# Optimization experiments

Measured on AMD Instinct MI355X. Metric: run time of the kernel, lower is better.

## Reference

```python
import jax, jax.numpy as jnp
import numpy as np

B, S, H = 4, 2048, 1024
EXP_BITS, SIG_BITS = 5, 10  # rmode=1 -> round-to-nearest


def quantize(x):
    """Simulated low-precision float quantization (LightChop-style) with STE.

    exp_bits exponent bits (bias = 2^(e-1)-1, exponent clamped -> subnormal
    handling falls out of the clamp), sig_bits significand bits, round-to-nearest.
    """
    bias = 2 ** (EXP_BITS - 1) - 1
    ax = jnp.abs(x)
    e = jnp.floor(jnp.log2(jnp.where(ax > 0, ax, 1.0)))
    e = jnp.clip(e, 1 - bias, bias)               # clamp to representable exponent range
    scale = jnp.exp2(e - SIG_BITS)                # ulp at this exponent
    q = jnp.round(x / scale) * scale              # round significand to SIG_BITS bits
    max_val = (2.0 - 2.0 ** (-SIG_BITS)) * 2.0 ** bias
    q = jnp.clip(q, -max_val, max_val)            # saturate overflow
    # straight-through estimator: forward = q, backward = identity
    return x + jax.lax.stop_gradient(q - x)


def setup_inputs() -> dict:
    key = jax.random.key(0)
    ks = jax.random.split(key, 7)
    w_scale = 1.0 / np.sqrt(H)
    return {
        "x": jax.random.normal(ks[0], (B, S, H), dtype=jnp.float32),
        "Wq": jax.random.normal(ks[1], (H, H), dtype=jnp.float32) * w_scale,
        "bq": jax.random.normal(ks[2], (H,), dtype=jnp.float32) * 0.01,
        "Wk": jax.random.normal(ks[3], (H, H), dtype=jnp.float32) * w_scale,
        "bk": jax.random.normal(ks[4], (H,), dtype=jnp.float32) * 0.01,
        "Wv": jax.random.normal(ks[5], (H, H), dtype=jnp.float32) * w_scale,
        "bv": jax.random.normal(ks[6], (H,), dtype=jnp.float32) * 0.01,
    }


def reference(x, Wq, bq, Wk, bk, Wv, bv):
    # nn.Linear: y = x @ W.T + b   (W stored [out, in])
    q = quantize(jnp.einsum("bsh,oh->bso", x, Wq) + bq)
    k = quantize(jnp.einsum("bsh,oh->bso", x, Wk) + bk)
    v = quantize(jnp.einsum("bsh,oh->bso", x, Wv) + bv)
    inv_sqrt_h = 1.0 / (H ** 0.5)
    scores = quantize(jnp.einsum("bsh,bth->bst", q, k) * inv_sqrt_h)  # [B,S,S]
    attn = quantize(jax.nn.softmax(scores, axis=-1))
    return jnp.einsum("bst,bth->bsh", attn, v)
```

## Files before the change

kernel.cpp:

```cpp
#include <hip/hip_runtime.h>
#include <hip/hip_fp16.h>

#define B_ 4
#define S_ 2048
#define H_ 1024
#define M_ (B_ * S_)

typedef _Float16 f16;
typedef _Float16 f16x8 __attribute__((ext_vector_type(8)));
typedef _Float16 f16x4 __attribute__((ext_vector_type(4)));
typedef float f32x4 __attribute__((ext_vector_type(4)));

typedef __attribute__((address_space(3))) unsigned int* lds_u32p;
typedef const __attribute__((address_space(1))) unsigned int* gbl_u32p;

__device__ __forceinline__ void stage16(const f16* g, f16* l) {
  __builtin_amdgcn_global_load_lds((gbl_u32p)g, (lds_u32p)l, 16, 0, 0);
}

__global__ __launch_bounds__(256) void downconvert_all(
    const float* __restrict__ x, const float* __restrict__ W0,
    const float* __restrict__ W1, const float* __restrict__ W2,
    f16* __restrict__ xh, f16* __restrict__ Wh) {
  const int b = blockIdx.x;
  const float* src;
  f16* dst;
  long i;
  if (b < M_ * H_ / 1024) {
    src = x; dst = xh;
    i = (long)b * 256 + threadIdx.x;
  } else {
    const int wb = b - M_ * H_ / 1024;
    const int sel = wb >> 10;
    src = sel == 0 ? W0 : (sel == 1 ? W1 : W2);
    dst = Wh + (long)sel * H_ * H_;
    i = (long)(wb & 1023) * 256 + threadIdx.x;
  }
  f32x4 v = ((const f32x4*)src)[i];
  f16x4 h;
#pragma unroll
  for (int c = 0; c < 4; c++) h[c] = (f16)v[c];
  ((f16x4*)dst)[i] = h;
}

__global__ __launch_bounds__(256, 2)
void qkv_gemm(const f16* __restrict__ xh, const f16* __restrict__ Wh,
              const float* __restrict__ bq, const float* __restrict__ bk,
              const float* __restrict__ bv, f16* __restrict__ qkv,
              f16* __restrict__ vT) {
  __shared__ __align__(16) f16 As[2 * 128 * 32];
  __shared__ __align__(16) f16 Bs[2 * 128 * 32];
  const int t = threadIdx.x;
  const int wave = t >> 6, lane = t & 63;
  const int quad = lane >> 4, l16 = lane & 15;
  const int wm = (wave & 1) * 64, wn = (wave >> 1) * 64;
  const int sel = blockIdx.y >> 3;
  const int ntile = (blockIdx.y & 7) * 128;
  const int mtile = blockIdx.x * 128;

  const f16* Ab = xh + (long)mtile * H_;
  const f16* Bb = Wh + (long)sel * H_ * H_ + (long)ntile * H_;

  const int r0 = t >> 2;
  const int c8 = (t & 3) * 8;

  f32x4 acc[4][4] = {};

  for (int k0 = 0; k0 < H_; k0 += 64) {
    __syncthreads();
    stage16(Ab + (long)r0 * H_ + k0 + c8,             As + t * 8);
    stage16(Ab + (long)(r0 + 64) * H_ + k0 + c8,      As + 2048 + t * 8);
    stage16(Ab + (long)r0 * H_ + k0 + 32 + c8,        As + 4096 + t * 8);
    stage16(Ab + (long)(r0 + 64) * H_ + k0 + 32 + c8, As + 6144 + t * 8);
    stage16(Bb + (long)r0 * H_ + k0 + c8,             Bs + t * 8);
    stage16(Bb + (long)(r0 + 64) * H_ + k0 + c8,      Bs + 2048 + t * 8);
    stage16(Bb + (long)r0 * H_ + k0 + 32 + c8,        Bs + 4096 + t * 8);
    stage16(Bb + (long)(r0 + 64) * H_ + k0 + 32 + c8, Bs + 6144 + t * 8);
    __syncthreads();
#pragma unroll
    for (int kk = 0; kk < 2; kk++) {
      f16x8 ah[4], bh[4];
#pragma unroll
      for (int i = 0; i < 4; i++) {
        ah[i] = *(const f16x8*)&As[kk * 4096 + (wm + i * 16 + l16) * 32 + quad * 8];
        bh[i] = *(const f16x8*)&Bs[kk * 4096 + (wn + i * 16 + l16) * 32 + quad * 8];
      }
#pragma unroll
      for (int i = 0; i < 4; i++)
#pragma unroll
        for (int j = 0; j < 4; j++)
          acc[i][j] = __builtin_amdgcn_mfma_f32_16x16x32_f16(ah[i], bh[j], acc[i][j], 0, 0, 0);
    }
  }

  const float* bias = sel == 0 ? bq : (sel == 1 ? bk : bv);
  if (sel == 2) {
#pragma unroll
    for (int j = 0; j < 4; j++) {
      int n = ntile + wn + j * 16 + l16;
      float bb = bias[n];
#pragma unroll
      for (int i = 0; i < 4; i++) {
        int m = mtile + wm + i * 16 + quad * 4;
        f16x4 pack;
#pragma unroll
        for (int r = 0; r < 4; r++) pack[r] = (f16)(acc[i][j][r] + bb);
        *(f16x4*)&vT[((long)(m >> 11) * H_ + n) * S_ + (m & 2047)] = pack;
      }
    }
  } else {
    f16* out = qkv + (long)sel * M_ * H_;
#pragma unroll
    for (int j = 0; j < 4; j++) {
      int n = ntile + wn + j * 16 + l16;
      float bb = bias[n];
#pragma unroll
      for (int i = 0; i < 4; i++) {
        int m = mtile + wm + i * 16 + quad * 4;
#pragma unroll
        for (int r = 0; r < 4; r++)
          out[(long)(m + r) * H_ + n] = (f16)(acc[i][j][r] + bb);
      }
    }
  }
}

template <int OUT_F16>
__global__ __launch_bounds__(256, 2)
void gemm_nt(const f16* __restrict__ A, const f16* __restrict__ Bm,
             void* __restrict__ C, int lda, int ldb, int ldc, int K,
             long sA, long sB, long sC, float alpha) {
  __shared__ __align__(16) f16 As[2 * 128 * 32];
  __shared__ __align__(16) f16 Bs[2 * 128 * 32];
  const int t = threadIdx.x;
  const int wave = t >> 6, lane = t & 63;
  const int quad = lane >> 4, l16 = lane & 15;
  const int wm = (wave & 1) * 64, wn = (wave >> 1) * 64;
  const f16* Ab = A + blockIdx.z * sA + (long)blockIdx.x * 128 * lda;
  const f16* Bb = Bm + blockIdx.z * sB + (long)blockIdx.y * 128 * ldb;
  const int r0 = t >> 2, c8 = (t & 3) * 8;
  f32x4 acc[4][4] = {};
  for (int k0 = 0; k0 < K; k0 += 64) {
    __syncthreads();
    stage16(Ab + (long)r0 * lda + k0 + c8,             As + t * 8);
    stage16(Ab + (long)(r0 + 64) * lda + k0 + c8,      As + 2048 + t * 8);
    stage16(Ab + (long)r0 * lda + k0 + 32 + c8,        As + 4096 + t * 8);
    stage16(Ab + (long)(r0 + 64) * lda + k0 + 32 + c8, As + 6144 + t * 8);
    stage16(Bb + (long)r0 * ldb + k0 + c8,             Bs + t * 8);
    stage16(Bb + (long)(r0 + 64) * ldb + k0 + c8,      Bs + 2048 + t * 8);
    stage16(Bb + (long)r0 * ldb + k0 + 32 + c8,        Bs + 4096 + t * 8);
    stage16(Bb + (long)(r0 + 64) * ldb + k0 + 32 + c8, Bs + 6144 + t * 8);
    __syncthreads();
#pragma unroll
    for (int kk = 0; kk < 2; kk++) {
      f16x8 af[4], bf[4];
#pragma unroll
      for (int i = 0; i < 4; i++) {
        af[i] = *(const f16x8*)&As[kk * 4096 + (wm + i * 16 + l16) * 32 + quad * 8];
        bf[i] = *(const f16x8*)&Bs[kk * 4096 + (wn + i * 16 + l16) * 32 + quad * 8];
      }
#pragma unroll
      for (int i = 0; i < 4; i++)
#pragma unroll
        for (int j = 0; j < 4; j++)
          acc[i][j] = __builtin_amdgcn_mfma_f32_16x16x32_f16(af[i], bf[j], acc[i][j], 0, 0, 0);
    }
  }
  const long mb = (long)blockIdx.x * 128 + wm;
  const long nb = (long)blockIdx.y * 128 + wn;
#pragma unroll
  for (int i = 0; i < 4; i++)
#pragma unroll
    for (int j = 0; j < 4; j++) {
      long m = mb + i * 16 + quad * 4;
      long n = nb + j * 16 + l16;
#pragma unroll
      for (int r = 0; r < 4; r++) {
        float v = acc[i][j][r] * alpha;
        if (OUT_F16)
          ((f16*)C)[blockIdx.z * sC + (m + r) * ldc + n] = (f16)v;
        else
          ((float*)C)[blockIdx.z * sC + (m + r) * ldc + n] = v;
      }
    }
}

__global__ __launch_bounds__(256) void softmax_q(f16* __restrict__ sc) {
  const long row = blockIdx.x;
  f16* p = sc + row * S_;
  const int t = threadIdx.x;
  const int wave = t >> 6, lane = t & 63;
  f16x8 v = ((const f16x8*)p)[t];
  float f[8];
  float m = -3.0e38f;
#pragma unroll
  for (int c = 0; c < 8; c++) { f[c] = (float)v[c]; m = fmaxf(m, f[c]); }
#pragma unroll
  for (int o = 32; o > 0; o >>= 1) m = fmaxf(m, __shfl_xor(m, o));
  __shared__ float redm[4], reds[4];
  if (lane == 0) redm[wave] = m;
  __syncthreads();
  m = fmaxf(fmaxf(redm[0], redm[1]), fmaxf(redm[2], redm[3]));
  float s = 0.f, e[8];
#pragma unroll
  for (int c = 0; c < 8; c++) { e[c] = __expf(f[c] - m); s += e[c]; }
#pragma unroll
  for (int o = 32; o > 0; o >>= 1) s += __shfl_xor(s, o);
  if (lane == 0) reds[wave] = s;
  __syncthreads();
  s = reds[0] + reds[1] + reds[2] + reds[3];
  float inv = 1.0f / s;
  f16x8 ov;
#pragma unroll
  for (int c = 0; c < 8; c++) ov[c] = (f16)(e[c] * inv);
  ((f16x8*)p)[t] = ov;
}

extern "C" void kernel_launch(void* const* d_in, const int* in_sizes, int n_in,
                              void* d_out, int out_size, void* d_ws, size_t ws_size,
                              hipStream_t stream) {
  (void)in_sizes; (void)n_in; (void)out_size; (void)ws_size;
  const float* x  = (const float*)d_in[0];
  const float* Wq = (const float*)d_in[1];
  const float* bq = (const float*)d_in[2];
  const float* Wk = (const float*)d_in[3];
  const float* bk = (const float*)d_in[4];
  const float* Wv = (const float*)d_in[5];
  const float* bv = (const float*)d_in[6];

  char* ws = (char*)d_ws;
  f16* xh  = (f16*)ws; ws += (size_t)M_ * H_ * 2;
  f16* Wh  = (f16*)ws; ws += (size_t)3 * H_ * H_ * 2;
  f16* qkv = (f16*)ws; ws += (size_t)2 * M_ * H_ * 2;
  f16* vT  = (f16*)ws; ws += (size_t)B_ * H_ * S_ * 2;
  f16* sc  = (f16*)ws; ws += (size_t)B_ * S_ * S_ * 2;

  downconvert_all<<<M_ * H_ / 1024 + 3 * H_ * H_ / 1024, 256, 0, stream>>>(
      x, Wq, Wk, Wv, xh, Wh);

  qkv_gemm<<<dim3(64, 24), 256, 0, stream>>>(xh, Wh, bq, bk, bv, qkv, vT);

  gemm_nt<1><<<dim3(16, 16, 4), 256, 0, stream>>>(
      qkv, qkv + (size_t)M_ * H_, sc, H_, H_, S_, H_,
      (long)S_ * H_, (long)S_ * H_, (long)S_ * S_, 0.03125f);

  softmax_q<<<M_, 256, 0, stream>>>(sc);

  gemm_nt<0><<<dim3(16, 8, 4), 256, 0, stream>>>(
      sc, vT, d_out, S_, S_, H_, S_,
      (long)S_ * S_, (long)H_ * S_, (long)S_ * H_, 1.0f);
}
```

Baseline: 248.3 us.

## Replace QKV and score GEMMs with 8-wave 256x256 multi-stage pipelined kernel

Introduces a templated 512-thread GEMM with 256x256 tiles, a 4-buffer LDS ring that prefetches three k-steps ahead via direct global-to-LDS loads, XOR-swizzled LDS layout, split barriers and setprio around MFMA bursts. It replaces both the QKV projection kernel and the QK^T score GEMM. The aim is to hide global load latency, raise data reuse per block and reduce LDS bank conflicts. In exchange it uses much more LDS and registers per block (acc[8][4]), which limits occupancy, and the larger tiles give fewer blocks (384 and 256), so wave quantization on the CUs may get worse.

```diff
diff --git a/kernel.cpp b/kernel.cpp
--- a/kernel.cpp
+++ b/kernel.cpp
@@ -43,83 +43,146 @@
   ((f16x4*)dst)[i] = h;
 }
 
-__global__ __launch_bounds__(256, 2)
-void qkv_gemm(const f16* __restrict__ xh, const f16* __restrict__ Wh,
-              const float* __restrict__ bq, const float* __restrict__ bk,
-              const float* __restrict__ bv, f16* __restrict__ qkv,
-              f16* __restrict__ vT) {
-  __shared__ __align__(16) f16 As[2 * 128 * 32];
-  __shared__ __align__(16) f16 Bs[2 * 128 * 32];
+template <int EPI>
+__global__ __launch_bounds__(512, 2)
+void gemm8p(const f16* __restrict__ A, const f16* __restrict__ Bm,
+            const float* __restrict__ bq, const float* __restrict__ bk,
+            const float* __restrict__ bv, f16* __restrict__ out,
+            f16* __restrict__ vT, float alpha) {
+  __shared__ __align__(16) f16 LA[4][256 * 32];
+  __shared__ __align__(16) f16 LB[4][256 * 32];
   const int t = threadIdx.x;
-  const int wave = t >> 6, lane = t & 63;
+  const int wv = t >> 6, lane = t & 63;
   const int quad = lane >> 4, l16 = lane & 15;
-  const int wm = (wave & 1) * 64, wn = (wave >> 1) * 64;
-  const int sel = blockIdx.y >> 3;
-  const int ntile = (blockIdx.y & 7) * 128;
-  const int mtile = blockIdx.x * 128;
-
-  const f16* Ab = xh + (long)mtile * H_;
-  const f16* Bb = Wh + (long)sel * H_ * H_ + (long)ntile * H_;
-
-  const int r0 = t >> 2;
-  const int c8 = (t & 3) * 8;
-
-  f32x4 acc[4][4] = {};
-
-  for (int k0 = 0; k0 < H_; k0 += 64) {
-    __syncthreads();
-    stage16(Ab + (long)r0 * H_ + k0 + c8,             As + t * 8);
-    stage16(Ab + (long)(r0 + 64) * H_ + k0 + c8,      As + 2048 + t * 8);
-    stage16(Ab + (long)r0 * H_ + k0 + 32 + c8,        As + 4096 + t * 8);
-    stage16(Ab + (long)(r0 + 64) * H_ + k0 + 32 + c8, As + 6144 + t * 8);
-    stage16(Bb + (long)r0 * H_ + k0 + c8,             Bs + t * 8);
-    stage16(Bb + (long)(r0 + 64) * H_ + k0 + c8,      Bs + 2048 + t * 8);
-    stage16(Bb + (long)r0 * H_ + k0 + 32 + c8,        Bs + 4096 + t * 8);
-    stage16(Bb + (long)(r0 + 64) * H_ + k0 + 32 + c8, Bs + 6144 + t * 8);
-    __syncthreads();
-#pragma unroll
-    for (int kk = 0; kk < 2; kk++) {
-      f16x8 ah[4], bh[4];
-#pragma unroll
-      for (int i = 0; i < 4; i++) {
-        ah[i] = *(const f16x8*)&As[kk * 4096 + (wm + i * 16 + l16) * 32 + quad * 8];
-        bh[i] = *(const f16x8*)&Bs[kk * 4096 + (wn + i * 16 + l16) * 32 + quad * 8];
-      }
-#pragma unroll
-      for (int i = 0; i < 4; i++)
-#pragma unroll
-        for (int j = 0; j < 4; j++)
-          acc[i][j] = __builtin_amdgcn_mfma_f32_16x16x32_f16(ah[i], bh[j], acc[i][j], 0, 0, 0);
-    }
-  }
-
-  const float* bias = sel == 0 ? bq : (sel == 1 ? bk : bv);
-  if (sel == 2) {
-#pragma unroll
-    for (int j = 0; j < 4; j++) {
-      int n = ntile + wn + j * 16 + l16;
-      float bb = bias[n];
-#pragma unroll
-      for (int i = 0; i < 4; i++) {
-        int m = mtile + wm + i * 16 + quad * 4;
-        f16x4 pack;
-#pragma unroll
-        for (int r = 0; r < 4; r++) pack[r] = (f16)(acc[i][j][r] + bb);
-        *(f16x4*)&vT[((long)(m >> 11) * H_ + n) * S_ + (m & 2047)] = pack;
-      }
-    }
+  const int wm = (wv >> 2) * 128;
+  const int wn = (wv & 3) * 64;
+
+  int bm, bn, sel = 0;
+  const f16 *Ab, *Bb;
+  if (EPI == 1) {
+    bm = blockIdx.x * 256;
+    sel = blockIdx.y >> 2;
+    bn = (blockIdx.y & 3) * 256;
+    Ab = A + (long)bm * H_;
+    Bb = Bm + (long)sel * H_ * H_ + (long)bn * H_;
   } else {
-    f16* out = qkv + (long)sel * M_ * H_;
-#pragma unroll
-    for (int j = 0; j < 4; j++) {
-      int n = ntile + wn + j * 16 + l16;
-      float bb = bias[n];
-#pragma unroll
-      for (int i = 0; i < 4; i++) {
-        int m = mtile + wm + i * 16 + quad * 4;
-#pragma unroll
-        for (int r = 0; r < 4; r++)
-          out[(long)(m + r) * H_ + n] = (f16)(acc[i][j][r] + bb);
+    bm = blockIdx.x * 256;
+    bn = blockIdx.y * 256;
+    Ab = A + (long)blockIdx.z * S_ * H_ + (long)bm * H_;
+    Bb = Bm + (long)blockIdx.z * S_ * H_ + (long)bn * H_;
+  }
+
+  const int srow = t >> 2;
+  const int sch = (t & 3) ^ ((srow >> 1) & 3);
+  const long goff = (long)srow * H_ + sch * 8;
+  const int loff = t * 8;
+
+  const int swz = quad ^ ((l16 >> 1) & 3);
+  const int aoff = (wm + l16) * 32 + swz * 8;
+  const int boff = (wn + l16) * 32 + swz * 8;
+
+  f32x4 acc[8][4] = {};
+
+#pragma unroll
+  for (int p = 0; p < 3; ++p) {
+    stage16(Ab + goff + p * 32, &LA[p][loff]);
+    stage16(Ab + goff + 128 * H_ + p * 32, &LA[p][loff + 4096]);
+    stage16(Bb + goff + p * 32, &LB[p][loff]);
+    stage16(Bb + goff + 128 * H_ + p * 32, &LB[p][loff + 4096]);
+  }
+
+#define KT_BODY(kt, VM, DO_STAGE)                                             \
+  {                                                                           \
+    asm volatile("s_waitcnt vmcnt(" #VM ")" ::: "memory");                    \
+    __builtin_amdgcn_s_barrier();                                             \
+    const int buf_ = (kt) & 3;                                                \
+    const f16* LAb = LA[buf_];                                                \
+    const f16* LBb = LB[buf_];                                                \
+    f16x8 af[4], bf[4], ag[4];                                                \
+    _Pragma("unroll") for (int mi = 0; mi < 4; ++mi)                          \
+        af[mi] = *(const f16x8*)&LAb[aoff + mi * 512];                        \
+    _Pragma("unroll") for (int ni = 0; ni < 4; ++ni)                          \
+        bf[ni] = *(const f16x8*)&LBb[boff + ni * 512];                        \
+    if (DO_STAGE) {                                                           \
+      stage16(Ab + goff + ((kt) + 3) * 32, &LA[((kt) + 3) & 3][loff]);        \
+      stage16(Ab + goff + 128 * H_ + ((kt) + 3) * 32,                         \
+              &LA[((kt) + 3) & 3][loff + 4096]);                              \
+    }                                                                         \
+    __builtin_amdgcn_s_barrier();                                             \
+    asm volatile("s_waitcnt lgkmcnt(0)" ::: "memory");                        \
+    __builtin_amdgcn_sched_barrier(0);                                        \
+    __builtin_amdgcn_s_setprio(1);                                            \
+    _Pragma("unroll") for (int mi = 0; mi < 4; ++mi)                          \
+        _Pragma("unroll") for (int ni = 0; ni < 4; ++ni)                      \
+            acc[mi][ni] = __builtin_amdgcn_mfma_f32_16x16x32_f16(             \
+                af[mi], bf[ni], acc[mi][ni], 0, 0, 0);                        \
+    __builtin_amdgcn_s_setprio(0);                                            \
+    _Pragma("unroll") for (int mi = 0; mi < 4; ++mi)                          \
+        ag[mi] = *(const f16x8*)&LAb[aoff + 2048 + mi * 512];                 \
+    if (DO_STAGE) {                                                           \
+      stage16(Bb + goff + ((kt) + 3) * 32, &LB[((kt) + 3) & 3][loff]);        \
+      stage16(Bb + goff + 128 * H_ + ((kt) + 3) * 32,                         \
+              &LB[((kt) + 3) & 3][loff + 4096]);                              \
+    }                                                                         \
+    __builtin_amdgcn_s_barrier();                                             \
+    asm volatile("s_waitcnt lgkmcnt(0)" ::: "memory");                        \
+    __builtin_amdgcn_sched_barrier(0);                                        \
+    __builtin_amdgcn_s_setprio(1);                                            \
+    _Pragma("unroll") for (int mi = 0; mi < 4; ++mi)                          \
+        _Pragma("unroll") for (int ni = 0; ni < 4; ++ni)                      \
+            acc[mi + 4][ni] = __builtin_amdgcn_mfma_f32_16x16x32_f16(         \
+                ag[mi], bf[ni], acc[mi + 4][ni], 0, 0, 0);                    \
+    __builtin_amdgcn_s_setprio(0);                                            \
+  }
+
+#pragma unroll 4
+  for (int kt = 0; kt < 29; ++kt) KT_BODY(kt, 8, 1)
+  KT_BODY(29, 8, 0)
+  KT_BODY(30, 4, 0)
+  KT_BODY(31, 0, 0)
+#undef KT_BODY
+
+  if (EPI == 0) {
+    f16* C = out + (long)blockIdx.z * S_ * S_;
+#pragma unroll
+    for (int mi = 0; mi < 8; ++mi)
+#pragma unroll
+      for (int ni = 0; ni < 4; ++ni) {
+        const long m = bm + wm + mi * 16 + quad * 4;
+        const long n = bn + wn + ni * 16 + l16;
+#pragma unroll
+        for (int r = 0; r < 4; ++r)
+          C[(m + r) * S_ + n] = (f16)(acc[mi][ni][r] * alpha);
+      }
+  } else {
+    const float* bias = sel == 0 ? bq : (sel == 1 ? bk : bv);
+    if (sel == 2) {
+#pragma unroll
+      for (int ni = 0; ni < 4; ++ni) {
+        const int n = bn + wn + ni * 16 + l16;
+        const float bb = bias[n];
+#pragma unroll
+        for (int mi = 0; mi < 8; ++mi) {
+          const int m = bm + wm + mi * 16 + quad * 4;
+          f16x4 pack;
+#pragma unroll
+          for (int r = 0; r < 4; ++r) pack[r] = (f16)(acc[mi][ni][r] + bb);
+          *(f16x4*)&vT[((long)(m >> 11) * H_ + n) * S_ + (m & 2047)] = pack;
+        }
+      }
+    } else {
+      f16* C = out + (long)sel * M_ * H_;
+#pragma unroll
+      for (int ni = 0; ni < 4; ++ni) {
+        const int n = bn + wn + ni * 16 + l16;
+        const float bb = bias[n];
+#pragma unroll
+        for (int mi = 0; mi < 8; ++mi) {
+          const long m = bm + wm + mi * 16 + quad * 4;
+#pragma unroll
+          for (int r = 0; r < 4; ++r)
+            C[(m + r) * H_ + n] = (f16)(acc[mi][ni][r] + bb);
+        }
       }
     }
   }
@@ -238,11 +301,12 @@
   downconvert_all<<<M_ * H_ / 1024 + 3 * H_ * H_ / 1024, 256, 0, stream>>>(
       x, Wq, Wk, Wv, xh, Wh);
 
-  qkv_gemm<<<dim3(64, 24), 256, 0, stream>>>(xh, Wh, bq, bk, bv, qkv, vT);
-
-  gemm_nt<1><<<dim3(16, 16, 4), 256, 0, stream>>>(
-      qkv, qkv + (size_t)M_ * H_, sc, H_, H_, S_, H_,
-      (long)S_ * H_, (long)S_ * H_, (long)S_ * S_, 0.03125f);
+  gemm8p<1><<<dim3(32, 12), 512, 0, stream>>>(
+      xh, Wh, bq, bk, bv, qkv, vT, 0.f);
+
+  gemm8p<0><<<dim3(8, 8, 4), 512, 0, stream>>>(
+      qkv, qkv + (size_t)M_ * H_, nullptr, nullptr, nullptr, sc, nullptr,
+      0.03125f);
 
   softmax_q<<<M_, 256, 0, stream>>>(sc);
 
```

Result: slower. 258.5 us (+4.1%).

## Unify GEMMs into triple-buffered pipelined kernel with swizzled LDS layout

Applied to the files above, without the earlier changes.

Replaces the separate QKV and NT GEMM kernels with one templated kernel. It uses a three-stage LDS ring buffer with a K-step of 32, so global-to-LDS loads for future tiles overlap the MFMA work on the current tile, paced by explicit vmcnt waits and raw barriers. LDS chunks are XOR-swizzled to reduce bank conflicts on the fragment reads, and MFMA sections run at raised wave priority. Occupancy is raised to 3 blocks per CU, which increases register pressure, and the hand-written waitcnt logic is fragile.

```diff
diff --git a/kernel.cpp b/kernel.cpp
--- a/kernel.cpp
+++ b/kernel.cpp
@@ -43,146 +43,176 @@
   ((f16x4*)dst)[i] = h;
 }
 
-__global__ __launch_bounds__(256, 2)
-void qkv_gemm(const f16* __restrict__ xh, const f16* __restrict__ Wh,
-              const float* __restrict__ bq, const float* __restrict__ bk,
-              const float* __restrict__ bv, f16* __restrict__ qkv,
-              f16* __restrict__ vT) {
-  __shared__ __align__(16) f16 As[2 * 128 * 32];
-  __shared__ __align__(16) f16 Bs[2 * 128 * 32];
+template <int KTOT, int EPI>
+__global__ __launch_bounds__(256, 3)
+void gemm_p(const f16* __restrict__ A, const f16* __restrict__ Bm,
+            void* __restrict__ Cout, f16* __restrict__ vT,
+            const float* __restrict__ bq, const float* __restrict__ bk,
+            const float* __restrict__ bv,
+            int lda, int ldb, int ldc, long sA, long sB, long sC,
+            float alpha) {
+  __shared__ __align__(16) f16 LA[3][128 * 32];
+  __shared__ __align__(16) f16 LB[3][128 * 32];
   const int t = threadIdx.x;
   const int wave = t >> 6, lane = t & 63;
   const int quad = lane >> 4, l16 = lane & 15;
   const int wm = (wave & 1) * 64, wn = (wave >> 1) * 64;
-  const int sel = blockIdx.y >> 3;
-  const int ntile = (blockIdx.y & 7) * 128;
-  const int mtile = blockIdx.x * 128;
-
-  const f16* Ab = xh + (long)mtile * H_;
-  const f16* Bb = Wh + (long)sel * H_ * H_ + (long)ntile * H_;
-
-  const int r0 = t >> 2;
-  const int c8 = (t & 3) * 8;
+
+  int sel = 0, ntile = 0, mtile = blockIdx.x * 128;
+  const f16 *Ab, *Bb;
+  if (EPI == 2) {
+    sel = blockIdx.y >> 3;
+    ntile = (blockIdx.y & 7) * 128;
+    Ab = A + (long)mtile * lda;
+    Bb = Bm + (long)sel * H_ * H_ + (long)ntile * ldb;
+  } else {
+    ntile = blockIdx.y * 128;
+    Ab = A + blockIdx.z * sA + (long)mtile * lda;
+    Bb = Bm + blockIdx.z * sB + (long)ntile * ldb;
+  }
+
+  const int srow = t >> 2;
+  const int sch = (t & 3) ^ ((srow >> 1) & 3);
+  const long ga = (long)srow * lda + sch * 8;
+  const long gb = (long)srow * ldb + sch * 8;
+
+  const int swz8 = (quad ^ ((l16 >> 1) & 3)) * 8;
+  const int aoff = (wm + l16) * 32 + swz8;
+  const int boff = (wn + l16) * 32 + swz8;
 
   f32x4 acc[4][4] = {};
 
-  for (int k0 = 0; k0 < H_; k0 += 64) {
-    __syncthreads();
-    stage16(Ab + (long)r0 * H_ + k0 + c8,             As + t * 8);
-    stage16(Ab + (long)(r0 + 64) * H_ + k0 + c8,      As + 2048 + t * 8);
-    stage16(Ab + (long)r0 * H_ + k0 + 32 + c8,        As + 4096 + t * 8);
-    stage16(Ab + (long)(r0 + 64) * H_ + k0 + 32 + c8, As + 6144 + t * 8);
-    stage16(Bb + (long)r0 * H_ + k0 + c8,             Bs + t * 8);
-    stage16(Bb + (long)(r0 + 64) * H_ + k0 + c8,      Bs + 2048 + t * 8);
-    stage16(Bb + (long)r0 * H_ + k0 + 32 + c8,        Bs + 4096 + t * 8);
-    stage16(Bb + (long)(r0 + 64) * H_ + k0 + 32 + c8, Bs + 6144 + t * 8);
-    __syncthreads();
-#pragma unroll
-    for (int kk = 0; kk < 2; kk++) {
-      f16x8 ah[4], bh[4];
-#pragma unroll
-      for (int i = 0; i < 4; i++) {
-        ah[i] = *(const f16x8*)&As[kk * 4096 + (wm + i * 16 + l16) * 32 + quad * 8];
-        bh[i] = *(const f16x8*)&Bs[kk * 4096 + (wn + i * 16 + l16) * 32 + quad * 8];
-      }
-#pragma unroll
-      for (int i = 0; i < 4; i++)
-#pragma unroll
-        for (int j = 0; j < 4; j++)
-          acc[i][j] = __builtin_amdgcn_mfma_f32_16x16x32_f16(ah[i], bh[j], acc[i][j], 0, 0, 0);
+#pragma unroll
+  for (int p = 0; p < 2; ++p) {
+    stage16(Ab + ga + p * 32,                    &LA[p][t * 8]);
+    stage16(Ab + ga + (long)64 * lda + p * 32,   &LA[p][t * 8 + 2048]);
+    stage16(Bb + gb + p * 32,                    &LB[p][t * 8]);
+    stage16(Bb + gb + (long)64 * ldb + p * 32,   &LB[p][t * 8 + 2048]);
+  }
+
+  constexpr int NT = KTOT / 32;
+  int rb = 0, sb = 2;
+  long kg = 64;
+
+#pragma unroll 3
+  for (int kt = 0; kt < NT - 2; ++kt) {
+    asm volatile("s_waitcnt vmcnt(4)" ::: "memory");
+    __builtin_amdgcn_s_barrier();
+    const f16* LAb = &LA[rb][0];
+    const f16* LBb = &LB[rb][0];
+    f16x8 af[4], bf[4];
+#pragma unroll
+    for (int i = 0; i < 4; ++i) {
+      af[i] = *(const f16x8*)&LAb[aoff + i * 512];
+      bf[i] = *(const f16x8*)&LBb[boff + i * 512];
     }
-  }
-
-  const float* bias = sel == 0 ? bq : (sel == 1 ? bk : bv);
-  if (sel == 2) {
-#pragma unroll
-    for (int j = 0; j < 4; j++) {
-      int n = ntile + wn + j * 16 + l16;
-      float bb = bias[n];
-#pragma unroll
-      for (int i = 0; i < 4; i++) {
-        int m = mtile + wm + i * 16 + quad * 4;
-        f16x4 pack;
-#pragma unroll
-        for (int r = 0; r < 4; r++) pack[r] = (f16)(acc[i][j][r] + bb);
-        *(f16x4*)&vT[((long)(m >> 11) * H_ + n) * S_ + (m & 2047)] = pack;
-      }
+    f16* sa = &LA[sb][0];
+    f16* sbb = &LB[sb][0];
+    stage16(Ab + ga + kg,                  sa + t * 8);
+    stage16(Ab + ga + (long)64 * lda + kg, sa + t * 8 + 2048);
+    stage16(Bb + gb + kg,                  sbb + t * 8);
+    stage16(Bb + gb + (long)64 * ldb + kg, sbb + t * 8 + 2048);
+    __builtin_amdgcn_s_barrier();
+    asm volatile("s_waitcnt lgkmcnt(0)" ::: "memory");
+    __builtin_amdgcn_sched_barrier(0);
+    __builtin_amdgcn_s_setprio(1);
+#pragma unroll
+    for (int i = 0; i < 4; ++i)
+#pragma unroll
+      for (int j = 0; j < 4; ++j)
+        acc[i][j] = __builtin_amdgcn_mfma_f32_16x16x32_f16(af[i], bf[j],
+                                                           acc[i][j], 0, 0, 0);
+    __builtin_amdgcn_s_setprio(0);
+    kg += 32;
+    rb = rb == 2 ? 0 : rb + 1;
+    sb = sb == 2 ? 0 : sb + 1;
+  }
+
+#pragma unroll
+  for (int tp = 0; tp < 2; ++tp) {
+    if (tp == 0)
+      asm volatile("s_waitcnt vmcnt(4)" ::: "memory");
+    else
+      asm volatile("s_waitcnt vmcnt(0)" ::: "memory");
+    __builtin_amdgcn_s_barrier();
+    const f16* LAb = &LA[rb][0];
+    const f16* LBb = &LB[rb][0];
+    f16x8 af[4], bf[4];
+#pragma unroll
+    for (int i = 0; i < 4; ++i) {
+      af[i] = *(const f16x8*)&LAb[aoff + i * 512];
+      bf[i] = *(const f16x8*)&LBb[boff + i * 512];
     }
+    __builtin_amdgcn_s_barrier();
+    asm volatile("s_waitcnt lgkmcnt(0)" ::: "memory");
+    __builtin_amdgcn_sched_barrier(0);
+    __builtin_amdgcn_s_setprio(1);
+#pragma unroll
+    for (int i = 0; i < 4; ++i)
+#pragma unroll
+      for (int j = 0; j < 4; ++j)
+        acc[i][j] = __builtin_amdgcn_mfma_f32_16x16x32_f16(af[i], bf[j],
+                                                           acc[i][j], 0, 0, 0);
+    __builtin_amdgcn_s_setprio(0);
+    rb = rb == 2 ? 0 : rb + 1;
+  }
+
+  if (EPI == 0) {
+    f16* C = (f16*)Cout + blockIdx.z * sC;
+#pragma unroll
+    for (int i = 0; i < 4; ++i)
+#pragma unroll
+      for (int j = 0; j < 4; ++j) {
+        const long m = mtile + wm + i * 16 + quad * 4;
+        const long n = ntile + wn + j * 16 + l16;
+#pragma unroll
+        for (int r = 0; r < 4; ++r)
+          C[(m + r) * ldc + n] = (f16)(acc[i][j][r] * alpha);
+      }
+  } else if (EPI == 1) {
+    float* C = (float*)Cout + blockIdx.z * sC;
+#pragma unroll
+    for (int i = 0; i < 4; ++i)
+#pragma unroll
+      for (int j = 0; j < 4; ++j) {
+        const long m = mtile + wm + i * 16 + quad * 4;
+        const long n = ntile + wn + j * 16 + l16;
+#pragma unroll
+        for (int r = 0; r < 4; ++r)
+          C[(m + r) * ldc + n] = acc[i][j][r] * alpha;
+      }
   } else {
-    f16* out = qkv + (long)sel * M_ * H_;
-#pragma unroll
-    for (int j = 0; j < 4; j++) {
-      int n = ntile + wn + j * 16 + l16;
-      float bb = bias[n];
-#pragma unroll
-      for (int i = 0; i < 4; i++) {
-        int m = mtile + wm + i * 16 + quad * 4;
-#pragma unroll
-        for (int r = 0; r < 4; r++)
-          out[(long)(m + r) * H_ + n] = (f16)(acc[i][j][r] + bb);
+    const float* bias = sel == 0 ? bq : (sel == 1 ? bk : bv);
+    if (sel == 2) {
+#pragma unroll
+      for (int j = 0; j < 4; ++j) {
+        const int n = ntile + wn + j * 16 + l16;
+        const float bb = bias[n];
+#pragma unroll
+        for (int i = 0; i < 4; ++i) {
+          const int m = mtile + wm + i * 16 + quad * 4;
+          f16x4 pack;
+#pragma unroll
+          for (int r = 0; r < 4; ++r) pack[r] = (f16)(acc[i][j][r] + bb);
+          *(f16x4*)&vT[((long)(m >> 11) * H_ + n) * S_ + (m & 2047)] = pack;
+        }
+      }
+    } else {
+      f16* C = (f16*)Cout + (long)sel * M_ * H_;
+#pragma unroll
+      for (int j = 0; j < 4; ++j) {
+        const int n = ntile + wn + j * 16 + l16;
+        const float bb = bias[n];
+#pragma unroll
+        for (int i = 0; i < 4; ++i) {
+          const long m = mtile + wm + i * 16 + quad * 4;
+#pragma unroll
+          for (int r = 0; r < 4; ++r)
+            C[(m + r) * ldc + n] = (f16)(acc[i][j][r] + bb);
+        }
       }
     }
   }
-}
-
-template <int OUT_F16>
-__global__ __launch_bounds__(256, 2)
-void gemm_nt(const f16* __restrict__ A, const f16* __restrict__ Bm,
-             void* __restrict__ C, int lda, int ldb, int ldc, int K,
-             long sA, long sB, long sC, float alpha) {
-  __shared__ __align__(16) f16 As[2 * 128 * 32];
-  __shared__ __align__(16) f16 Bs[2 * 128 * 32];
-  const int t = threadIdx.x;
-  const int wave = t >> 6, lane = t & 63;
-  const int quad = lane >> 4, l16 = lane & 15;
-  const int wm = (wave & 1) * 64, wn = (wave >> 1) * 64;
-  const f16* Ab = A + blockIdx.z * sA + (long)blockIdx.x * 128 * lda;
-  const f16* Bb = Bm + blockIdx.z * sB + (long)blockIdx.y * 128 * ldb;
-  const int r0 = t >> 2, c8 = (t & 3) * 8;
-  f32x4 acc[4][4] = {};
-  for (int k0 = 0; k0 < K; k0 += 64) {
-    __syncthreads();
-    stage16(Ab + (long)r0 * lda + k0 + c8,             As + t * 8);
-    stage16(Ab + (long)(r0 + 64) * lda + k0 + c8,      As + 2048 + t * 8);
-    stage16(Ab + (long)r0 * lda + k0 + 32 + c8,        As + 4096 + t * 8);
-    stage16(Ab + (long)(r0 + 64) * lda + k0 + 32 + c8, As + 6144 + t * 8);
-    stage16(Bb + (long)r0 * ldb + k0 + c8,             Bs + t * 8);
-    stage16(Bb + (long)(r0 + 64) * ldb + k0 + c8,      Bs + 2048 + t * 8);
-    stage16(Bb + (long)r0 * ldb + k0 + 32 + c8,        Bs + 4096 + t * 8);
-    stage16(Bb + (long)(r0 + 64) * ldb + k0 + 32 + c8, Bs + 6144 + t * 8);
-    __syncthreads();
-#pragma unroll
-    for (int kk = 0; kk < 2; kk++) {
-      f16x8 af[4], bf[4];
-#pragma unroll
-      for (int i = 0; i < 4; i++) {
-        af[i] = *(const f16x8*)&As[kk * 4096 + (wm + i * 16 + l16) * 32 + quad * 8];
-        bf[i] = *(const f16x8*)&Bs[kk * 4096 + (wn + i * 16 + l16) * 32 + quad * 8];
-      }
-#pragma unroll
-      for (int i = 0; i < 4; i++)
-#pragma unroll
-        for (int j = 0; j < 4; j++)
-          acc[i][j] = __builtin_amdgcn_mfma_f32_16x16x32_f16(af[i], bf[j], acc[i][j], 0, 0, 0);
-    }
-  }
-  const long mb = (long)blockIdx.x * 128 + wm;
-  const long nb = (long)blockIdx.y * 128 + wn;
-#pragma unroll
-  for (int i = 0; i < 4; i++)
-#pragma unroll
-    for (int j = 0; j < 4; j++) {
-      long m = mb + i * 16 + quad * 4;
-      long n = nb + j * 16 + l16;
-#pragma unroll
-      for (int r = 0; r < 4; r++) {
-        float v = acc[i][j][r] * alpha;
-        if (OUT_F16)
-          ((f16*)C)[blockIdx.z * sC + (m + r) * ldc + n] = (f16)v;
-        else
-          ((float*)C)[blockIdx.z * sC + (m + r) * ldc + n] = v;
-      }
-    }
 }
 
 __global__ __launch_bounds__(256) void softmax_q(f16* __restrict__ sc) {
@@ -238,15 +268,16 @@
   downconvert_all<<<M_ * H_ / 1024 + 3 * H_ * H_ / 1024, 256, 0, stream>>>(
       x, Wq, Wk, Wv, xh, Wh);
 
-  qkv_gemm<<<dim3(64, 24), 256, 0, stream>>>(xh, Wh, bq, bk, bv, qkv, vT);
-
-  gemm_nt<1><<<dim3(16, 16, 4), 256, 0, stream>>>(
-      qkv, qkv + (size_t)M_ * H_, sc, H_, H_, S_, H_,
-      (long)S_ * H_, (long)S_ * H_, (long)S_ * S_, 0.03125f);
+  gemm_p<1024, 2><<<dim3(64, 24), 256, 0, stream>>>(
+      xh, Wh, qkv, vT, bq, bk, bv, H_, H_, H_, 0, 0, 0, 0.f);
+
+  gemm_p<1024, 0><<<dim3(16, 16, 4), 256, 0, stream>>>(
+      qkv, qkv + (size_t)M_ * H_, sc, nullptr, nullptr, nullptr, nullptr,
+      H_, H_, S_, (long)S_ * H_, (long)S_ * H_, (long)S_ * S_, 0.03125f);
 
   softmax_q<<<M_, 256, 0, stream>>>(sc);
 
-  gemm_nt<0><<<dim3(16, 8, 4), 256, 0, stream>>>(
-      sc, vT, d_out, S_, S_, H_, S_,
-      (long)S_ * S_, (long)H_ * S_, (long)S_ * H_, 1.0f);
-}
+  gemm_p<2048, 1><<<dim3(16, 8, 4), 256, 0, stream>>>(
+      sc, vT, d_out, nullptr, nullptr, nullptr, nullptr,
+      S_, S_, H_, (long)S_ * S_, (long)H_ * S_, (long)S_ * H_, 1.0f);
+}
```

Result: slower. 262.2 us (+5.6%).

## Use 2-wave 128x64-per-wave GEMM tiles with swizzled LDS for QKV and scores

Applied to the files above, without the earlier changes.

Replaces the QKV projection kernel and the scores GEMM with one templated kernel. It runs 128 threads per block, and each wave computes a 128x64 output tile with 8x4 MFMA accumulators, so every B fragment loaded from LDS is reused across more MFMAs. LDS chunks are XOR-swizzled on the global-to-LDS store and the fragment reads to reduce bank conflicts. In exchange, each wave holds many more accumulator registers and each CU has fewer waves to hide latency.

```diff
diff --git a/kernel.cpp b/kernel.cpp
--- a/kernel.cpp
+++ b/kernel.cpp
@@ -43,83 +43,125 @@
   ((f16x4*)dst)[i] = h;
 }
 
-__global__ __launch_bounds__(256, 2)
-void qkv_gemm(const f16* __restrict__ xh, const f16* __restrict__ Wh,
-              const float* __restrict__ bq, const float* __restrict__ bk,
-              const float* __restrict__ bv, f16* __restrict__ qkv,
-              f16* __restrict__ vT) {
-  __shared__ __align__(16) f16 As[2 * 128 * 32];
-  __shared__ __align__(16) f16 Bs[2 * 128 * 32];
+template <int KTOT, int EPI>
+__global__ __launch_bounds__(128, 2)
+void gemm_f(const f16* __restrict__ A, const f16* __restrict__ Bm,
+            void* __restrict__ Cout, f16* __restrict__ vT,
+            const float* __restrict__ bq, const float* __restrict__ bk,
+            const float* __restrict__ bv,
+            int lda, int ldb, int ldc, long sA, long sB, long sC,
+            float alpha) {
+  __shared__ __align__(16) f16 As[2][128 * 32];
+  __shared__ __align__(16) f16 Bs[2][128 * 32];
   const int t = threadIdx.x;
   const int wave = t >> 6, lane = t & 63;
   const int quad = lane >> 4, l16 = lane & 15;
-  const int wm = (wave & 1) * 64, wn = (wave >> 1) * 64;
-  const int sel = blockIdx.y >> 3;
-  const int ntile = (blockIdx.y & 7) * 128;
-  const int mtile = blockIdx.x * 128;
-
-  const f16* Ab = xh + (long)mtile * H_;
-  const f16* Bb = Wh + (long)sel * H_ * H_ + (long)ntile * H_;
-
-  const int r0 = t >> 2;
-  const int c8 = (t & 3) * 8;
-
-  f32x4 acc[4][4] = {};
-
-  for (int k0 = 0; k0 < H_; k0 += 64) {
-    __syncthreads();
-    stage16(Ab + (long)r0 * H_ + k0 + c8,             As + t * 8);
-    stage16(Ab + (long)(r0 + 64) * H_ + k0 + c8,      As + 2048 + t * 8);
-    stage16(Ab + (long)r0 * H_ + k0 + 32 + c8,        As + 4096 + t * 8);
-    stage16(Ab + (long)(r0 + 64) * H_ + k0 + 32 + c8, As + 6144 + t * 8);
-    stage16(Bb + (long)r0 * H_ + k0 + c8,             Bs + t * 8);
-    stage16(Bb + (long)(r0 + 64) * H_ + k0 + c8,      Bs + 2048 + t * 8);
-    stage16(Bb + (long)r0 * H_ + k0 + 32 + c8,        Bs + 4096 + t * 8);
-    stage16(Bb + (long)(r0 + 64) * H_ + k0 + 32 + c8, Bs + 6144 + t * 8);
-    __syncthreads();
-#pragma unroll
-    for (int kk = 0; kk < 2; kk++) {
-      f16x8 ah[4], bh[4];
-#pragma unroll
-      for (int i = 0; i < 4; i++) {
-        ah[i] = *(const f16x8*)&As[kk * 4096 + (wm + i * 16 + l16) * 32 + quad * 8];
-        bh[i] = *(const f16x8*)&Bs[kk * 4096 + (wn + i * 16 + l16) * 32 + quad * 8];
-      }
-#pragma unroll
-      for (int i = 0; i < 4; i++)
-#pragma unroll
-        for (int j = 0; j < 4; j++)
-          acc[i][j] = __builtin_amdgcn_mfma_f32_16x16x32_f16(ah[i], bh[j], acc[i][j], 0, 0, 0);
-    }
-  }
-
-  const float* bias = sel == 0 ? bq : (sel == 1 ? bk : bv);
-  if (sel == 2) {
-#pragma unroll
-    for (int j = 0; j < 4; j++) {
-      int n = ntile + wn + j * 16 + l16;
-      float bb = bias[n];
-#pragma unroll
-      for (int i = 0; i < 4; i++) {
-        int m = mtile + wm + i * 16 + quad * 4;
-        f16x4 pack;
-#pragma unroll
-        for (int r = 0; r < 4; r++) pack[r] = (f16)(acc[i][j][r] + bb);
-        *(f16x4*)&vT[((long)(m >> 11) * H_ + n) * S_ + (m & 2047)] = pack;
-      }
-    }
+  const int wn = wave * 64;
+
+  int sel = 0, ntile = 0, mtile = blockIdx.x * 128;
+  const f16 *Ab, *Bb;
+  if (EPI == 2) {
+    sel = blockIdx.y >> 3;
+    ntile = (blockIdx.y & 7) * 128;
+    Ab = A + (long)mtile * lda;
+    Bb = Bm + (long)sel * H_ * H_ + (long)ntile * ldb;
   } else {
-    f16* out = qkv + (long)sel * M_ * H_;
-#pragma unroll
-    for (int j = 0; j < 4; j++) {
-      int n = ntile + wn + j * 16 + l16;
-      float bb = bias[n];
-#pragma unroll
-      for (int i = 0; i < 4; i++) {
-        int m = mtile + wm + i * 16 + quad * 4;
-#pragma unroll
-        for (int r = 0; r < 4; r++)
-          out[(long)(m + r) * H_ + n] = (f16)(acc[i][j][r] + bb);
+    ntile = blockIdx.y * 128;
+    Ab = A + blockIdx.z * sA + (long)mtile * lda;
+    Bb = Bm + blockIdx.z * sB + (long)ntile * ldb;
+  }
+
+  const int srow = t >> 2;
+  const int sch = (t & 3) ^ ((t >> 3) & 3);
+  const long gaBase = (long)srow * lda + sch * 8;
+  const long gbBase = (long)srow * ldb + sch * 8;
+
+  const int swz8 = (quad ^ ((l16 >> 1) & 3)) * 8;
+  const int aoff = l16 * 32 + swz8;
+  const int boff = (wn + l16) * 32 + swz8;
+
+  f32x4 acc[8][4] = {};
+
+  for (int k0 = 0; k0 < KTOT; k0 += 64) {
+    __syncthreads();
+#pragma unroll
+    for (int j = 0; j < 4; ++j) {
+      const long rA = gaBase + (long)(32 * j) * lda + k0;
+      const long rB = gbBase + (long)(32 * j) * ldb + k0;
+      stage16(Ab + rA,      &As[0][j * 1024 + t * 8]);
+      stage16(Ab + rA + 32, &As[1][j * 1024 + t * 8]);
+      stage16(Bb + rB,      &Bs[0][j * 1024 + t * 8]);
+      stage16(Bb + rB + 32, &Bs[1][j * 1024 + t * 8]);
+    }
+    __syncthreads();
+#pragma unroll
+    for (int kk = 0; kk < 2; ++kk) {
+      f16x8 af[4], bf[4];
+#pragma unroll
+      for (int i = 0; i < 4; ++i) {
+        af[i] = *(const f16x8*)&As[kk][aoff + i * 512];
+        bf[i] = *(const f16x8*)&Bs[kk][boff + i * 512];
+      }
+#pragma unroll
+      for (int i = 0; i < 4; ++i)
+#pragma unroll
+        for (int j2 = 0; j2 < 4; ++j2)
+          acc[i][j2] = __builtin_amdgcn_mfma_f32_16x16x32_f16(
+              af[i], bf[j2], acc[i][j2], 0, 0, 0);
+      f16x8 ag[4];
+#pragma unroll
+      for (int i = 0; i < 4; ++i)
+        ag[i] = *(const f16x8*)&As[kk][aoff + (i + 4) * 512];
+#pragma unroll
+      for (int i = 0; i < 4; ++i)
+#pragma unroll
+        for (int j2 = 0; j2 < 4; ++j2)
+          acc[i + 4][j2] = __builtin_amdgcn_mfma_f32_16x16x32_f16(
+              ag[i], bf[j2], acc[i + 4][j2], 0, 0, 0);
+    }
+  }
+
+  if (EPI == 0) {
+    f16* C = (f16*)Cout + blockIdx.z * sC;
+#pragma unroll
+    for (int mi = 0; mi < 8; ++mi)
+#pragma unroll
+      for (int ni = 0; ni < 4; ++ni) {
+        const long m = mtile + mi * 16 + quad * 4;
+        const long n = ntile + wn + ni * 16 + l16;
+#pragma unroll
+        for (int r = 0; r < 4; ++r)
+          C[(m + r) * ldc + n] = (f16)(acc[mi][ni][r] * alpha);
+      }
+  } else {
+    const float* bias = sel == 0 ? bq : (sel == 1 ? bk : bv);
+    if (sel == 2) {
+#pragma unroll
+      for (int ni = 0; ni < 4; ++ni) {
+        const int n = ntile + wn + ni * 16 + l16;
+        const float bb = bias[n];
+#pragma unroll
+        for (int mi = 0; mi < 8; ++mi) {
+          const int m = mtile + mi * 16 + quad * 4;
+          f16x4 pack;
+#pragma unroll
+          for (int r = 0; r < 4; ++r) pack[r] = (f16)(acc[mi][ni][r] + bb);
+          *(f16x4*)&vT[((long)(m >> 11) * H_ + n) * S_ + (m & 2047)] = pack;
+        }
+      }
+    } else {
+      f16* C = (f16*)Cout + (long)sel * M_ * H_;
+#pragma unroll
+      for (int ni = 0; ni < 4; ++ni) {
+        const int n = ntile + wn + ni * 16 + l16;
+        const float bb = bias[n];
+#pragma unroll
+        for (int mi = 0; mi < 8; ++mi) {
+          const long m = mtile + mi * 16 + quad * 4;
+#pragma unroll
+          for (int r = 0; r < 4; ++r)
+            C[(m + r) * ldc + n] = (f16)(acc[mi][ni][r] + bb);
+        }
       }
     }
   }
@@ -238,11 +280,12 @@
   downconvert_all<<<M_ * H_ / 1024 + 3 * H_ * H_ / 1024, 256, 0, stream>>>(
       x, Wq, Wk, Wv, xh, Wh);
 
-  qkv_gemm<<<dim3(64, 24), 256, 0, stream>>>(xh, Wh, bq, bk, bv, qkv, vT);
-
-  gemm_nt<1><<<dim3(16, 16, 4), 256, 0, stream>>>(
-      qkv, qkv + (size_t)M_ * H_, sc, H_, H_, S_, H_,
-      (long)S_ * H_, (long)S_ * H_, (long)S_ * S_, 0.03125f);
+  gemm_f<1024, 2><<<dim3(64, 24), 128, 0, stream>>>(
+      xh, Wh, qkv, vT, bq, bk, bv, H_, H_, H_, 0, 0, 0, 0.f);
+
+  gemm_f<1024, 0><<<dim3(16, 16, 4), 128, 0, stream>>>(
+      qkv, qkv + (size_t)M_ * H_, sc, nullptr, nullptr, nullptr, nullptr,
+      H_, H_, S_, (long)S_ * H_, (long)S_ * H_, (long)S_ * S_, 0.03125f);
 
   softmax_q<<<M_, 256, 0, stream>>>(sc);
 
```

After: 256.2 us. 3.2% more time.
